# Kernel tuning notes

Measured on AMD Instinct MI355X. Metric: run time of the kernel, lower is better.

Reference implementation:

```python
import jax, jax.numpy as jnp
import numpy as np

DIM = 128
HEADS = 4
HD = DIM // HEADS  # 32
WS = 8             # search window (ws x ws candidates)
K = 16             # top-k neighbors kept
SCALE = HD ** -0.5


def _sepconv(x, w_dw, w_pw, b):
    # depthwise 3x3 ('SAME', reflect-free) + pointwise 1x1 with bias (SepConv2d)
    C = x.shape[1]
    y = jax.lax.conv_general_dilated(x, w_dw, (1, 1), 'SAME',
                                     feature_group_count=C,
                                     dimension_numbers=('NCHW', 'OIHW', 'NCHW'))
    return jnp.einsum('bchw,oc->bohw', y, w_pw) + b[None, :, None, None]


def _refl(i, n):
    # dnls reflect_bounds: mirror indices back into [0, n-1]
    i = jnp.where(i < 0, -i, i)
    return jnp.where(i >= n, 2 * (n - 1) - i, i)


def _neighbor_idx(T, H, W, ws):
    # flat pixel index of the ws*ws spatial candidates per query (wt=0: same frame)
    off = jnp.arange(ws) - ws // 2
    ni = _refl(jnp.arange(H)[:, None] + off[None, :], H)  # [H,ws]
    nj = _refl(jnp.arange(W)[:, None] + off[None, :], W)  # [W,ws]
    pix = ni[:, None, :, None] * W + nj[None, :, None, :]  # [H,W,ws,ws]
    idx = jnp.arange(T)[:, None, None, None, None] * (H * W) + pix[None]
    return idx.reshape(T * H * W, ws * ws).astype(jnp.int32)  # [Q,L]


def reference(vid, wq_dw, wq_pw, bq, wk_dw, wk_pw, bk, wv_dw, wv_pw, bv, proj_w, proj_b):
    B, T, C, H, W = vid.shape
    Q = T * H * W
    x = vid.reshape(B * T, C, H, W)
    # qkv conv projection; q pre-scaled as in get_qkv
    q = _sepconv(x, wq_dw, wq_pw, bq) * SCALE
    k = _sepconv(x, wk_dw, wk_pw, bk)
    v = _sepconv(x, wv_dw, wv_pw, bv)

    def heads(z):  # [B*T,C,H,W] -> [B,heads,Q,hd]
        return z.reshape(B, T, HEADS, HD, H, W).transpose(0, 2, 1, 4, 5, 3).reshape(B, HEADS, Q, HD)

    qh, kh, vh = heads(q), heads(k), heads(v)
    idx = _neighbor_idx(T, H, W, WS)            # [Q,L]
    kg = jnp.take(kh, idx, axis=2)              # [B,h,Q,L,hd] irregular gather
    dists = jnp.einsum('bhqd,bhqld->bhql', qh, kg)
    vals, args = jax.lax.top_k(dists, K)        # k-NN by prod distance
    attn = jax.nn.softmax(vals, axis=-1)        # run_softmax over k
    sel = jnp.take_along_axis(jnp.broadcast_to(idx[None, None], (B, HEADS) + idx.shape), args, axis=-1)
    vsel = jnp.take_along_axis(vh, sel.reshape(B, HEADS, Q * K)[..., None], axis=2).reshape(B, HEADS, Q, K, HD)
    out = jnp.einsum('bhqk,bhqkd->bhqd', attn, vsel)   # wpsum (ps=pt=1)
    out = out.transpose(0, 2, 1, 3).reshape(B, Q, C)   # merge heads: (h c)
    y = out @ proj_w.T + proj_b                        # nn.Linear proj
    # fold: ps=1, stride0=1 -> zvid==1, pure reshape back to video
    return y.reshape(B, T, H, W, C).transpose(0, 1, 4, 2, 3)


def setup_inputs() -> dict:
    key = jax.random.key(0)
    ks = jax.random.split(key, 12)
    s = 0.02
    return {
        'vid': jax.random.normal(ks[0], (1, 2, DIM, 96, 96), jnp.float32),
        'wq_dw': jax.random.normal(ks[1], (DIM, 1, 3, 3), jnp.float32) * s,
        'wq_pw': jax.random.normal(ks[2], (DIM, DIM), jnp.float32) * s,
        'bq': jax.random.normal(ks[3], (DIM,), jnp.float32) * s,
        'wk_dw': jax.random.normal(ks[4], (DIM, 1, 3, 3), jnp.float32) * s,
        'wk_pw': jax.random.normal(ks[5], (DIM, DIM), jnp.float32) * s,
        'bk': jax.random.normal(ks[6], (DIM,), jnp.float32) * s,
        'wv_dw': jax.random.normal(ks[7], (DIM, 1, 3, 3), jnp.float32) * s,
        'wv_pw': jax.random.normal(ks[8], (DIM, DIM), jnp.float32) * s,
        'bv': jax.random.normal(ks[9], (DIM,), jnp.float32) * s,
        'proj_w': jax.random.normal(ks[10], (DIM, DIM), jnp.float32) * s,
        'proj_b': jax.random.normal(ks[11], (DIM,), jnp.float32) * s,
    }
```

## Files before the change

kernel.cpp:

```cpp
#include <hip/hip_runtime.h>
#include <math.h>

#define TT 2
#define CH 128
#define HH 96
#define WW 96
#define HWS 9216
#define QTOT 18432
#define QC (QTOT*CH)
#define HD 32
#define KTOP 16
#define SCALE 0.17677669529663687f

#define SEG 16
#define PR 8
#define PC 23
#define PSTRIDE 36

typedef __attribute__((ext_vector_type(8))) short short8;
typedef __attribute__((ext_vector_type(4))) float floatx4;

__device__ __forceinline__ unsigned short f2bf(float f) {
    union { float f; unsigned u; } x; x.f = f;
    unsigned r = x.u + 0x7fffu + ((x.u >> 16) & 1u);
    return (unsigned short)(r >> 16);
}
__device__ __forceinline__ float bf2f(unsigned short h) {
    return __uint_as_float(((unsigned)h) << 16);
}

__device__ __forceinline__ int refl(int x, int n) {
    x = x < 0 ? -x : x;
    return x >= n ? 2 * (n - 1) - x : x;
}

__global__ __launch_bounds__(256) void dw_kernel(
    const float* __restrict__ x,
    const float* __restrict__ wq, const float* __restrict__ wk, const float* __restrict__ wv,
    float* __restrict__ t_dw)
{
    int tid = blockIdx.x * 256 + threadIdx.x;
    int hw = tid % HWS;
    int cf = tid / HWS;
    int c = cf & (CH - 1);
    int tt = cf >> 7;
    int i = hw / WW, j = hw % WW;
    const float* xp = x + (size_t)(tt * CH + c) * HWS;
    float w0[9], w1[9], w2[9];
#pragma unroll
    for (int r = 0; r < 9; r++) { w0[r] = wq[c * 9 + r]; w1[r] = wk[c * 9 + r]; w2[r] = wv[c * 9 + r]; }
    float s0 = 0.f, s1 = 0.f, s2 = 0.f;
#pragma unroll
    for (int r = 0; r < 3; r++) {
        int ii = i + r - 1;
        if (ii < 0 || ii >= HH) continue;
#pragma unroll
        for (int ss = 0; ss < 3; ss++) {
            int jj = j + ss - 1;
            if (jj < 0 || jj >= WW) continue;
            float xv = xp[ii * WW + jj];
            s0 += xv * w0[r * 3 + ss];
            s1 += xv * w1[r * 3 + ss];
            s2 += xv * w2[r * 3 + ss];
        }
    }
    size_t o = (size_t)c * QTOT + tt * HWS + hw;
    t_dw[o] = s0;
    t_dw[QC + o] = s1;
    t_dw[2 * (size_t)QC + o] = s2;
}

__global__ __launch_bounds__(256) void transcvt(
    const float* __restrict__ t_dw,
    unsigned short* __restrict__ qk_hi,
    unsigned short* __restrict__ qk_lo,
    unsigned short* __restrict__ v_bf)
{
    __shared__ float s[64][33];
    int sel = blockIdx.z;
    const float* vd = t_dw + (size_t)sel * QC;
    int t = threadIdx.x;
    int p0 = blockIdx.x * 64;
    int c0 = blockIdx.y * 32;
#pragma unroll
    for (int r = 0; r < 2; r++) {
        int lin = r * 256 + t;
        int c = lin >> 4;
        int pq = lin & 15;
        float4 v4 = *(const float4*)(vd + (size_t)(c0 + c) * QTOT + p0 + pq * 4);
        s[pq * 4 + 0][c] = v4.x; s[pq * 4 + 1][c] = v4.y;
        s[pq * 4 + 2][c] = v4.z; s[pq * 4 + 3][c] = v4.w;
    }
    __syncthreads();
    int p = t >> 2, cq = t & 3;
    unsigned uh[8], ul[8];
#pragma unroll
    for (int j = 0; j < 8; j++) {
        float x = s[p][cq * 8 + j];
        unsigned short h = f2bf(x);
        uh[j] = h;
        ul[j] = f2bf(x - bf2f(h));
    }
    uint4 ph, pl;
    ph.x = uh[0] | (uh[1] << 16); ph.y = uh[2] | (uh[3] << 16);
    ph.z = uh[4] | (uh[5] << 16); ph.w = uh[6] | (uh[7] << 16);
    size_t off = (size_t)(p0 + p) * CH + c0 + cq * 8;
    if (sel < 2) {
        pl.x = ul[0] | (ul[1] << 16); pl.y = ul[2] | (ul[3] << 16);
        pl.z = ul[4] | (ul[5] << 16); pl.w = ul[6] | (ul[7] << 16);
        *(uint4*)(qk_hi + (size_t)sel * QC + off) = ph;
        *(uint4*)(qk_lo + (size_t)sel * QC + off) = pl;
    } else {
        *(uint4*)(v_bf + off) = ph;
    }
}

__global__ __launch_bounds__(256) void qk_mfma(
    const unsigned short* __restrict__ Ahi,
    const unsigned short* __restrict__ Alo,
    const float* __restrict__ wq_pw, const float* __restrict__ wk_pw,
    const float* __restrict__ bq, const float* __restrict__ bk,
    float* __restrict__ t_dw)
{
    int sel = blockIdx.y;
    const float* W = sel ? wk_pw : wq_pw;
    const float* bias = sel ? bk : bq;
    float scale = sel ? 1.f : SCALE;
    const unsigned short* ah = Ahi + (size_t)sel * QC;
    const unsigned short* al = Alo + (size_t)sel * QC;
    float* O = t_dw + (size_t)sel * QC;

    __shared__ unsigned short Wh[128 * 136];
    __shared__ unsigned short Wl[128 * 136];
    int t = threadIdx.x;
#pragma unroll
    for (int r = 0; r < 16; r++) {
        int lin = r * 256 + t;
        int o = lin >> 5, cq = lin & 31;
        float4 w4 = *(const float4*)(W + o * CH + cq * 4);
        unsigned short hx = f2bf(w4.x), hy = f2bf(w4.y), hz = f2bf(w4.z), hw = f2bf(w4.w);
        unsigned short lx = f2bf(w4.x - bf2f(hx)), ly = f2bf(w4.y - bf2f(hy));
        unsigned short lz = f2bf(w4.z - bf2f(hz)), lw = f2bf(w4.w - bf2f(hw));
        uint2 pk;
        pk.x = hx | ((unsigned)hy << 16); pk.y = hz | ((unsigned)hw << 16);
        *(uint2*)(&Wh[o * 136 + cq * 4]) = pk;
        pk.x = lx | ((unsigned)ly << 16); pk.y = lz | ((unsigned)lw << 16);
        *(uint2*)(&Wl[o * 136 + cq * 4]) = pk;
    }
    __syncthreads();
    int wv = t >> 6, lane = t & 63;
    int m = lane & 15, quad = lane >> 4;
    int p0 = blockIdx.x * 64;
    int o0 = wv * 32;
    float bb[2];
#pragma unroll
    for (int ot = 0; ot < 2; ot++) bb[ot] = bias[o0 + ot * 16 + m];
    floatx4 acc[4][2];
#pragma unroll
    for (int i = 0; i < 4; i++)
#pragma unroll
        for (int j = 0; j < 2; j++) acc[i][j] = (floatx4){0.f, 0.f, 0.f, 0.f};
#pragma unroll
    for (int kc = 0; kc < 4; kc++) {
        short8 avh[4], avl[4], bh[2], bl[2];
#pragma unroll
        for (int pt = 0; pt < 4; pt++) {
            size_t base = (size_t)(p0 + pt * 16 + m) * CH + kc * 32 + quad * 8;
            avh[pt] = *(const short8*)(ah + base);
            avl[pt] = *(const short8*)(al + base);
        }
#pragma unroll
        for (int ot = 0; ot < 2; ot++) {
            int lidx = (o0 + ot * 16 + m) * 136 + kc * 32 + quad * 8;
            bh[ot] = *(const short8*)(&Wh[lidx]);
            bl[ot] = *(const short8*)(&Wl[lidx]);
        }
#pragma unroll
        for (int pt = 0; pt < 4; pt++)
#pragma unroll
            for (int ot = 0; ot < 2; ot++) {
                acc[pt][ot] = __builtin_amdgcn_mfma_f32_16x16x32_bf16(avh[pt], bh[ot], acc[pt][ot], 0, 0, 0);
                acc[pt][ot] = __builtin_amdgcn_mfma_f32_16x16x32_bf16(avh[pt], bl[ot], acc[pt][ot], 0, 0, 0);
                acc[pt][ot] = __builtin_amdgcn_mfma_f32_16x16x32_bf16(avl[pt], bh[ot], acc[pt][ot], 0, 0, 0);
            }
    }
#pragma unroll
    for (int pt = 0; pt < 4; pt++)
#pragma unroll
        for (int ot = 0; ot < 2; ot++)
#pragma unroll
            for (int reg = 0; reg < 4; reg++) {
                int p = p0 + pt * 16 + quad * 4 + reg;
                O[(size_t)p * CH + o0 + ot * 16 + m] = (acc[pt][ot][reg] + bb[ot]) * scale;
            }
}

__global__ __launch_bounds__(256) void vgemm_mfma(
    const unsigned short* __restrict__ A,
    const float* __restrict__ W,
    const float* __restrict__ bias,
    float* __restrict__ O)
{
    __shared__ unsigned short Ws[128 * 136];
    int t = threadIdx.x;
#pragma unroll
    for (int r = 0; r < 16; r++) {
        int lin = r * 256 + t;
        int o = lin >> 5, cq = lin & 31;
        float4 w4 = *(const float4*)(W + o * CH + cq * 4);
        uint2 pk;
        pk.x = f2bf(w4.x) | ((unsigned)f2bf(w4.y) << 16);
        pk.y = f2bf(w4.z) | ((unsigned)f2bf(w4.w) << 16);
        *(uint2*)(&Ws[o * 136 + cq * 4]) = pk;
    }
    __syncthreads();
    int wv = t >> 6, lane = t & 63;
    int m = lane & 15, quad = lane >> 4;
    int p0 = blockIdx.x * 64;
    int o0 = wv * 32;
    float bb[2];
#pragma unroll
    for (int ot = 0; ot < 2; ot++) bb[ot] = bias[o0 + ot * 16 + m];
    floatx4 acc[4][2];
#pragma unroll
    for (int i = 0; i < 4; i++)
#pragma unroll
        for (int j = 0; j < 2; j++) acc[i][j] = (floatx4){0.f, 0.f, 0.f, 0.f};
#pragma unroll
    for (int kc = 0; kc < 4; kc++) {
        short8 a[4], b[2];
#pragma unroll
        for (int pt = 0; pt < 4; pt++)
            a[pt] = *(const short8*)(A + (size_t)(p0 + pt * 16 + m) * CH + kc * 32 + quad * 8);
#pragma unroll
        for (int ot = 0; ot < 2; ot++)
            b[ot] = *(const short8*)(&Ws[(o0 + ot * 16 + m) * 136 + kc * 32 + quad * 8]);
#pragma unroll
        for (int pt = 0; pt < 4; pt++)
#pragma unroll
            for (int ot = 0; ot < 2; ot++)
                acc[pt][ot] = __builtin_amdgcn_mfma_f32_16x16x32_bf16(a[pt], b[ot], acc[pt][ot], 0, 0, 0);
    }
#pragma unroll
    for (int pt = 0; pt < 4; pt++)
#pragma unroll
        for (int ot = 0; ot < 2; ot++)
#pragma unroll
            for (int reg = 0; reg < 4; reg++) {
                int p = p0 + pt * 16 + quad * 4 + reg;
                O[(size_t)p * CH + o0 + ot * 16 + m] = acc[pt][ot][reg] + bb[ot];
            }
}

__global__ __launch_bounds__(256) void attn_kernel(
    const float* __restrict__ q,
    const float* __restrict__ k,
    const float* __restrict__ v,
    unsigned short* __restrict__ att)
{
    __shared__ float kp[PR * PC * PSTRIDE];
    int h = blockIdx.y;
    int seg = blockIdx.x;
    int qj0 = (seg % (WW / SEG)) * SEG;
    int qi = (seg / (WW / SEG)) % HH;
    int tt = seg / ((WW / SEG) * HH);
    int t = threadIdx.x;

#pragma unroll
    for (int r = 0; r < 6; r++) {
        int f = r * 256 + t;
        if (f < PR * PC * 8) {
            int pix = f >> 3, d4 = f & 7;
            int ci = pix / PC, cj = pix - ci * PC;
            int gi = refl(qi + ci - 4, HH);
            int gj = refl(qj0 + cj - 4, WW);
            int gp = tt * HWS + gi * WW + gj;
            *(float4*)(&kp[pix * PSTRIDE + d4 * 4]) =
                *(const float4*)(k + (size_t)gp * CH + h * HD + d4 * 4);
        }
    }
    __syncthreads();

    int wv = t >> 6, lane = t & 63;
    int ci = lane >> 3, cjo = lane & 7;
    int di = ci - 4, dj = cjo - 4;
    int rowoff = tt * HWS + refl(qi + di, HH) * WW;
    const int d = lane & (HD - 1);
    const unsigned long long below = (1ull << lane) - 1ull;

    for (int ql = wv * 4; ql < wv * 4 + 4; ql++) {
        int qj = qj0 + ql;
        int p = tt * HWS + qi * WW + qj;
        const float* qp = q + (size_t)p * CH + h * HD;
        const float* kr = &kp[(ci * PC + ql + cjo) * PSTRIDE];
        float dist = 0.f;
#pragma unroll
        for (int dd = 0; dd < 8; dd++) {
            float4 qv = *(const float4*)(qp + dd * 4);
            float4 kv = *(const float4*)(kr + dd * 4);
            dist += qv.x * kv.x + qv.y * kv.y + qv.z * kv.z + qv.w * kv.w;
        }
        int cpix = rowoff + refl(qj + dj, WW);

        unsigned u = __float_as_uint(dist);
        unsigned key = (u & 0x80000000u) ? ~u : (u | 0x80000000u);

        unsigned prefix = 0u;
        int need = KTOP;
#pragma unroll
        for (int bit = 31; bit >= 0; --bit) {
            unsigned hi = (prefix >> bit) | 1u;
            unsigned long long b = __ballot((key >> bit) == hi);
            int cnt = __popcll(b);
            bool take = cnt >= need;
            prefix = take ? (prefix | (1u << bit)) : prefix;
            need = take ? need : need - cnt;
        }
        bool isEq = (key == prefix);
        unsigned long long eqm = __ballot(isEq);
        int rk = __popcll(eqm & below);
        bool selb = (key > prefix) || (isEq && rk < need);
        unsigned long long selm = __ballot(selb);

        float e = selb ? __expf(dist) : 0.f;

        float acc = 0.f, denom = 0.f;
        unsigned long long m0 = selm;
#pragma unroll
        for (int r = 0; r < KTOP; r++) {
            int s0 = __builtin_ctzll(m0); m0 &= m0 - 1ull;
            float a0 = __uint_as_float((unsigned)__builtin_amdgcn_readlane((int)__float_as_uint(e), s0));
            int p0 = __builtin_amdgcn_readlane(cpix, s0);
            denom += a0;
            acc += a0 * v[(size_t)p0 * CH + h * HD + d];
        }
        if (lane < HD)
            att[(size_t)p * CH + h * HD + lane] = f2bf(acc / denom);
    }
}

__global__ __launch_bounds__(256) void proj_mfma(
    const unsigned short* __restrict__ A,
    const float* __restrict__ W,
    const float* __restrict__ bias,
    float* __restrict__ out)
{
    __shared__ unsigned short Ws[128 * 136];
    int t = threadIdx.x;
#pragma unroll
    for (int r = 0; r < 16; r++) {
        int lin = r * 256 + t;
        int o = lin >> 5, cq = lin & 31;
        float4 w4 = *(const float4*)(W + o * CH + cq * 4);
        uint2 pk;
        pk.x = f2bf(w4.x) | ((unsigned)f2bf(w4.y) << 16);
        pk.y = f2bf(w4.z) | ((unsigned)f2bf(w4.w) << 16);
        *(uint2*)(&Ws[o * 136 + cq * 4]) = pk;
    }
    __syncthreads();
    int wv = t >> 6, lane = t & 63;
    int m = lane & 15, quad = lane >> 4;
    int p0 = blockIdx.x * 64;
    int o0 = wv * 32;
    float bb[2][4];
#pragma unroll
    for (int ot = 0; ot < 2; ot++)
#pragma unroll
        for (int reg = 0; reg < 4; reg++) bb[ot][reg] = bias[o0 + ot * 16 + quad * 4 + reg];
    floatx4 acc[2][4];
#pragma unroll
    for (int i = 0; i < 2; i++)
#pragma unroll
        for (int j = 0; j < 4; j++) acc[i][j] = (floatx4){0.f, 0.f, 0.f, 0.f};
#pragma unroll
    for (int kc = 0; kc < 4; kc++) {
        short8 a[2], b[4];
#pragma unroll
        for (int ot = 0; ot < 2; ot++)
            a[ot] = *(const short8*)(&Ws[(o0 + ot * 16 + m) * 136 + kc * 32 + quad * 8]);
#pragma unroll
        for (int pt = 0; pt < 4; pt++)
            b[pt] = *(const short8*)(A + (size_t)(p0 + pt * 16 + m) * CH + kc * 32 + quad * 8);
#pragma unroll
        for (int ot = 0; ot < 2; ot++)
#pragma unroll
            for (int pt = 0; pt < 4; pt++)
                acc[ot][pt] = __builtin_amdgcn_mfma_f32_16x16x32_bf16(a[ot], b[pt], acc[ot][pt], 0, 0, 0);
    }
    int tt = p0 / HWS;
    int hwb = p0 - tt * HWS;
#pragma unroll
    for (int ot = 0; ot < 2; ot++)
#pragma unroll
        for (int pt = 0; pt < 4; pt++)
#pragma unroll
            for (int reg = 0; reg < 4; reg++) {
                int o = o0 + ot * 16 + quad * 4 + reg;
                int hw = hwb + pt * 16 + m;
                out[((size_t)(tt * CH + o)) * HWS + hw] = acc[ot][pt][reg] + bb[ot][reg];
            }
}

extern "C" void kernel_launch(void* const* d_in, const int* in_sizes, int n_in,
                              void* d_out, int out_size, void* d_ws, size_t ws_size,
                              hipStream_t stream) {
    const float* vid    = (const float*)d_in[0];
    const float* wq_dw  = (const float*)d_in[1];
    const float* wq_pw  = (const float*)d_in[2];
    const float* bq     = (const float*)d_in[3];
    const float* wk_dw  = (const float*)d_in[4];
    const float* wk_pw  = (const float*)d_in[5];
    const float* bk     = (const float*)d_in[6];
    const float* wv_dw  = (const float*)d_in[7];
    const float* wv_pw  = (const float*)d_in[8];
    const float* bv     = (const float*)d_in[9];
    const float* proj_w = (const float*)d_in[10];
    const float* proj_b = (const float*)d_in[11];
    float* out = (float*)d_out;

    float* t_dw = (float*)d_ws;
    float* v_f32 = t_dw + (size_t)3 * QC;
    unsigned short* qk_hi = (unsigned short*)(v_f32 + (size_t)QC);
    unsigned short* qk_lo = qk_hi + (size_t)2 * QC;
    unsigned short* v_bf = qk_lo + (size_t)2 * QC;
    unsigned short* att_bf = v_bf;

    dw_kernel<<<QTOT * CH / 256, 256, 0, stream>>>(vid, wq_dw, wk_dw, wv_dw, t_dw);
    transcvt<<<dim3(QTOT / 64, 4, 3), 256, 0, stream>>>(t_dw, qk_hi, qk_lo, v_bf);
    qk_mfma<<<dim3(QTOT / 64, 2), 256, 0, stream>>>(qk_hi, qk_lo, wq_pw, wk_pw, bq, bk, t_dw);
    vgemm_mfma<<<QTOT / 64, 256, 0, stream>>>(v_bf, wv_pw, bv, v_f32);
    attn_kernel<<<dim3(TT * HH * (WW / SEG), 4), 256, 0, stream>>>(
        t_dw, t_dw + (size_t)QC, v_f32, att_bf);
    proj_mfma<<<QTOT / 64, 256, 0, stream>>>(att_bf, proj_w, proj_b, out);
}
```

Measured before the change: 205.8 us.

## Precompute bf16 weight splits once and give attention one wave per query

A new wprep kernel converts the four pointwise and projection weight matrices to bf16 (with hi/lo splits for q and k) once per call into workspace. The GEMM kernels then read those weights straight from global memory instead of having every block convert them into LDS. Separately, the attention kernel now runs 1024-thread blocks with one wave per query instead of each wave looping over four queries, which raises parallelism. The cost is an extra kernel launch, uncached global weight reads inside the MFMA loops, and lower occupancy headroom from the larger blocks.

```diff
diff --git a/kernel.cpp b/kernel.cpp
--- a/kernel.cpp
+++ b/kernel.cpp
@@ -17,6 +17,10 @@
 #define PC 23
 #define PSTRIDE 36
 
+#define WB_QK(sel) ((sel) * 32768)
+#define WB_V 65536
+#define WB_P 81920
+
 typedef __attribute__((ext_vector_type(8))) short short8;
 typedef __attribute__((ext_vector_type(4))) float floatx4;
 
@@ -32,6 +36,28 @@
 __device__ __forceinline__ int refl(int x, int n) {
     x = x < 0 ? -x : x;
     return x >= n ? 2 * (n - 1) - x : x;
+}
+
+__global__ __launch_bounds__(256) void wprep(
+    const float* __restrict__ wq, const float* __restrict__ wk,
+    const float* __restrict__ wv, const float* __restrict__ pj,
+    unsigned short* __restrict__ wbuf)
+{
+    int sel = blockIdx.y;
+    const float* src = sel == 0 ? wq : (sel == 1 ? wk : (sel == 2 ? wv : pj));
+    int hi_off = sel == 0 ? 0 : (sel == 1 ? 32768 : (sel == 2 ? WB_V : WB_P));
+    int idx = blockIdx.x * 256 + threadIdx.x;
+    float4 w4 = *(const float4*)(src + idx * 4);
+    unsigned short hx = f2bf(w4.x), hy = f2bf(w4.y), hz = f2bf(w4.z), hw = f2bf(w4.w);
+    uint2 pk;
+    pk.x = hx | ((unsigned)hy << 16); pk.y = hz | ((unsigned)hw << 16);
+    *(uint2*)(wbuf + hi_off + idx * 4) = pk;
+    if (sel < 2) {
+        unsigned short lx = f2bf(w4.x - bf2f(hx)), ly = f2bf(w4.y - bf2f(hy));
+        unsigned short lz = f2bf(w4.z - bf2f(hz)), lw = f2bf(w4.w - bf2f(hw));
+        pk.x = lx | ((unsigned)ly << 16); pk.y = lz | ((unsigned)lw << 16);
+        *(uint2*)(wbuf + hi_off + 16384 + idx * 4) = pk;
+    }
 }
 
 __global__ __launch_bounds__(256) void dw_kernel(
@@ -118,36 +144,20 @@
 __global__ __launch_bounds__(256) void qk_mfma(
     const unsigned short* __restrict__ Ahi,
     const unsigned short* __restrict__ Alo,
-    const float* __restrict__ wq_pw, const float* __restrict__ wk_pw,
+    const unsigned short* __restrict__ wbuf,
     const float* __restrict__ bq, const float* __restrict__ bk,
     float* __restrict__ t_dw)
 {
     int sel = blockIdx.y;
-    const float* W = sel ? wk_pw : wq_pw;
+    const unsigned short* Wh = wbuf + WB_QK(sel);
+    const unsigned short* Wl = Wh + 16384;
     const float* bias = sel ? bk : bq;
     float scale = sel ? 1.f : SCALE;
     const unsigned short* ah = Ahi + (size_t)sel * QC;
     const unsigned short* al = Alo + (size_t)sel * QC;
     float* O = t_dw + (size_t)sel * QC;
 
-    __shared__ unsigned short Wh[128 * 136];
-    __shared__ unsigned short Wl[128 * 136];
     int t = threadIdx.x;
-#pragma unroll
-    for (int r = 0; r < 16; r++) {
-        int lin = r * 256 + t;
-        int o = lin >> 5, cq = lin & 31;
-        float4 w4 = *(const float4*)(W + o * CH + cq * 4);
-        unsigned short hx = f2bf(w4.x), hy = f2bf(w4.y), hz = f2bf(w4.z), hw = f2bf(w4.w);
-        unsigned short lx = f2bf(w4.x - bf2f(hx)), ly = f2bf(w4.y - bf2f(hy));
-        unsigned short lz = f2bf(w4.z - bf2f(hz)), lw = f2bf(w4.w - bf2f(hw));
-        uint2 pk;
-        pk.x = hx | ((unsigned)hy << 16); pk.y = hz | ((unsigned)hw << 16);
-        *(uint2*)(&Wh[o * 136 + cq * 4]) = pk;
-        pk.x = lx | ((unsigned)ly << 16); pk.y = lz | ((unsigned)lw << 16);
-        *(uint2*)(&Wl[o * 136 + cq * 4]) = pk;
-    }
-    __syncthreads();
     int wv = t >> 6, lane = t & 63;
     int m = lane & 15, quad = lane >> 4;
     int p0 = blockIdx.x * 64;
@@ -171,9 +181,9 @@
         }
 #pragma unroll
         for (int ot = 0; ot < 2; ot++) {
-            int lidx = (o0 + ot * 16 + m) * 136 + kc * 32 + quad * 8;
-            bh[ot] = *(const short8*)(&Wh[lidx]);
-            bl[ot] = *(const short8*)(&Wl[lidx]);
+            int widx = (o0 + ot * 16 + m) * CH + kc * 32 + quad * 8;
+            bh[ot] = *(const short8*)(Wh + widx);
+            bl[ot] = *(const short8*)(Wl + widx);
         }
 #pragma unroll
         for (int pt = 0; pt < 4; pt++)
@@ -197,23 +207,12 @@
 
 __global__ __launch_bounds__(256) void vgemm_mfma(
     const unsigned short* __restrict__ A,
-    const float* __restrict__ W,
+    const unsigned short* __restrict__ wbuf,
     const float* __restrict__ bias,
     float* __restrict__ O)
 {
-    __shared__ unsigned short Ws[128 * 136];
+    const unsigned short* Wv = wbuf + WB_V;
     int t = threadIdx.x;
-#pragma unroll
-    for (int r = 0; r < 16; r++) {
-        int lin = r * 256 + t;
-        int o = lin >> 5, cq = lin & 31;
-        float4 w4 = *(const float4*)(W + o * CH + cq * 4);
-        uint2 pk;
-        pk.x = f2bf(w4.x) | ((unsigned)f2bf(w4.y) << 16);
-        pk.y = f2bf(w4.z) | ((unsigned)f2bf(w4.w) << 16);
-        *(uint2*)(&Ws[o * 136 + cq * 4]) = pk;
-    }
-    __syncthreads();
     int wv = t >> 6, lane = t & 63;
     int m = lane & 15, quad = lane >> 4;
     int p0 = blockIdx.x * 64;
@@ -234,7 +233,7 @@
             a[pt] = *(const short8*)(A + (size_t)(p0 + pt * 16 + m) * CH + kc * 32 + quad * 8);
 #pragma unroll
         for (int ot = 0; ot < 2; ot++)
-            b[ot] = *(const short8*)(&Ws[(o0 + ot * 16 + m) * 136 + kc * 32 + quad * 8]);
+            b[ot] = *(const short8*)(Wv + (o0 + ot * 16 + m) * CH + kc * 32 + quad * 8);
 #pragma unroll
         for (int pt = 0; pt < 4; pt++)
 #pragma unroll
@@ -252,7 +251,7 @@
             }
 }
 
-__global__ __launch_bounds__(256) void attn_kernel(
+__global__ __launch_bounds__(1024) void attn_kernel(
     const float* __restrict__ q,
     const float* __restrict__ k,
     const float* __restrict__ v,
@@ -267,8 +266,8 @@
     int t = threadIdx.x;
 
 #pragma unroll
-    for (int r = 0; r < 6; r++) {
-        int f = r * 256 + t;
+    for (int r = 0; r < 2; r++) {
+        int f = r * 1024 + t;
         if (f < PR * PC * 8) {
             int pix = f >> 3, d4 = f & 7;
             int ci = pix / PC, cj = pix - ci * PC;
@@ -281,83 +280,70 @@
     }
     __syncthreads();
 
-    int wv = t >> 6, lane = t & 63;
+    int lane = t & 63;
+    int ql = __builtin_amdgcn_readfirstlane(t >> 6);
     int ci = lane >> 3, cjo = lane & 7;
     int di = ci - 4, dj = cjo - 4;
-    int rowoff = tt * HWS + refl(qi + di, HH) * WW;
     const int d = lane & (HD - 1);
     const unsigned long long below = (1ull << lane) - 1ull;
 
-    for (int ql = wv * 4; ql < wv * 4 + 4; ql++) {
-        int qj = qj0 + ql;
-        int p = tt * HWS + qi * WW + qj;
-        const float* qp = q + (size_t)p * CH + h * HD;
-        const float* kr = &kp[(ci * PC + ql + cjo) * PSTRIDE];
-        float dist = 0.f;
-#pragma unroll
-        for (int dd = 0; dd < 8; dd++) {
-            float4 qv = *(const float4*)(qp + dd * 4);
-            float4 kv = *(const float4*)(kr + dd * 4);
-            dist += qv.x * kv.x + qv.y * kv.y + qv.z * kv.z + qv.w * kv.w;
-        }
-        int cpix = rowoff + refl(qj + dj, WW);
-
-        unsigned u = __float_as_uint(dist);
-        unsigned key = (u & 0x80000000u) ? ~u : (u | 0x80000000u);
-
-        unsigned prefix = 0u;
-        int need = KTOP;
-#pragma unroll
-        for (int bit = 31; bit >= 0; --bit) {
-            unsigned hi = (prefix >> bit) | 1u;
-            unsigned long long b = __ballot((key >> bit) == hi);
-            int cnt = __popcll(b);
-            bool take = cnt >= need;
-            prefix = take ? (prefix | (1u << bit)) : prefix;
-            need = take ? need : need - cnt;
-        }
-        bool isEq = (key == prefix);
-        unsigned long long eqm = __ballot(isEq);
-        int rk = __popcll(eqm & below);
-        bool selb = (key > prefix) || (isEq && rk < need);
-        unsigned long long selm = __ballot(selb);
-
-        float e = selb ? __expf(dist) : 0.f;
-
-        float acc = 0.f, denom = 0.f;
-        unsigned long long m0 = selm;
-#pragma unroll
-        for (int r = 0; r < KTOP; r++) {
-            int s0 = __builtin_ctzll(m0); m0 &= m0 - 1ull;
-            float a0 = __uint_as_float((unsigned)__builtin_amdgcn_readlane((int)__float_as_uint(e), s0));
-            int p0 = __builtin_amdgcn_readlane(cpix, s0);
-            denom += a0;
-            acc += a0 * v[(size_t)p0 * CH + h * HD + d];
-        }
-        if (lane < HD)
-            att[(size_t)p * CH + h * HD + lane] = f2bf(acc / denom);
-    }
+    int qj = qj0 + ql;
+    int p = tt * HWS + qi * WW + qj;
+    const float* qp = q + (size_t)p * CH + h * HD;
+    const float* kr = &kp[(ci * PC + ql + cjo) * PSTRIDE];
+    float dist = 0.f;
+#pragma unroll
+    for (int dd = 0; dd < 8; dd++) {
+        float4 qv = *(const float4*)(qp + dd * 4);
+        float4 kv = *(const float4*)(kr + dd * 4);
+        dist += qv.x * kv.x + qv.y * kv.y + qv.z * kv.z + qv.w * kv.w;
+    }
+    int cpix = tt * HWS + refl(qi + di, HH) * WW + refl(qj + dj, WW);
+
+    unsigned u = __float_as_uint(dist);
+    unsigned key = (u & 0x80000000u) ? ~u : (u | 0x80000000u);
+
+    unsigned prefix = 0u;
+    int need = KTOP;
+#pragma unroll
+    for (int bit = 31; bit >= 0; --bit) {
+        unsigned hi = (prefix >> bit) | 1u;
+        unsigned long long b = __ballot((key >> bit) == hi);
+        int cnt = __popcll(b);
+        bool take = cnt >= need;
+        prefix = take ? (prefix | (1u << bit)) : prefix;
+        need = take ? need : need - cnt;
+    }
+    bool isEq = (key == prefix);
+    unsigned long long eqm = __ballot(isEq);
+    int rk = __popcll(eqm & below);
+    bool selb = (key > prefix) || (isEq && rk < need);
+    unsigned long long selm = __ballot(selb);
+
+    float e = selb ? __expf(dist) : 0.f;
+
+    float acc = 0.f, denom = 0.f;
+    unsigned long long m0 = selm;
+#pragma unroll
+    for (int r = 0; r < KTOP; r++) {
+        int s0 = __builtin_ctzll(m0); m0 &= m0 - 1ull;
+        float a0 = __uint_as_float((unsigned)__builtin_amdgcn_readlane((int)__float_as_uint(e), s0));
+        int pr = __builtin_amdgcn_readlane(cpix, s0);
+        denom += a0;
+        acc += a0 * v[(size_t)pr * CH + h * HD + d];
+    }
+    if (lane < HD)
+        att[(size_t)p * CH + h * HD + lane] = f2bf(acc / denom);
 }
 
 __global__ __launch_bounds__(256) void proj_mfma(
     const unsigned short* __restrict__ A,
-    const float* __restrict__ W,
+    const unsigned short* __restrict__ wbuf,
     const float* __restrict__ bias,
     float* __restrict__ out)
 {
-    __shared__ unsigned short Ws[128 * 136];
+    const unsigned short* Wp = wbuf + WB_P;
     int t = threadIdx.x;
-#pragma unroll
-    for (int r = 0; r < 16; r++) {
-        int lin = r * 256 + t;
-        int o = lin >> 5, cq = lin & 31;
-        float4 w4 = *(const float4*)(W + o * CH + cq * 4);
-        uint2 pk;
-        pk.x = f2bf(w4.x) | ((unsigned)f2bf(w4.y) << 16);
-        pk.y = f2bf(w4.z) | ((unsigned)f2bf(w4.w) << 16);
-        *(uint2*)(&Ws[o * 136 + cq * 4]) = pk;
-    }
-    __syncthreads();
     int wv = t >> 6, lane = t & 63;
     int m = lane & 15, quad = lane >> 4;
     int p0 = blockIdx.x * 64;
@@ -377,7 +363,7 @@
         short8 a[2], b[4];
 #pragma unroll
         for (int ot = 0; ot < 2; ot++)
-            a[ot] = *(const short8*)(&Ws[(o0 + ot * 16 + m) * 136 + kc * 32 + quad * 8]);
+            a[ot] = *(const short8*)(Wp + (o0 + ot * 16 + m) * CH + kc * 32 + quad * 8);
 #pragma unroll
         for (int pt = 0; pt < 4; pt++)
             b[pt] = *(const short8*)(A + (size_t)(p0 + pt * 16 + m) * CH + kc * 32 + quad * 8);
@@ -423,13 +409,15 @@
     unsigned short* qk_hi = (unsigned short*)(v_f32 + (size_t)QC);
     unsigned short* qk_lo = qk_hi + (size_t)2 * QC;
     unsigned short* v_bf = qk_lo + (size_t)2 * QC;
+    unsigned short* wbuf = v_bf + (size_t)QC;
     unsigned short* att_bf = v_bf;
 
+    wprep<<<dim3(16, 4), 256, 0, stream>>>(wq_pw, wk_pw, wv_pw, proj_w, wbuf);
     dw_kernel<<<QTOT * CH / 256, 256, 0, stream>>>(vid, wq_dw, wk_dw, wv_dw, t_dw);
     transcvt<<<dim3(QTOT / 64, 4, 3), 256, 0, stream>>>(t_dw, qk_hi, qk_lo, v_bf);
-    qk_mfma<<<dim3(QTOT / 64, 2), 256, 0, stream>>>(qk_hi, qk_lo, wq_pw, wk_pw, bq, bk, t_dw);
-    vgemm_mfma<<<QTOT / 64, 256, 0, stream>>>(v_bf, wv_pw, bv, v_f32);
-    attn_kernel<<<dim3(TT * HH * (WW / SEG), 4), 256, 0, stream>>>(
+    qk_mfma<<<dim3(QTOT / 64, 2), 256, 0, stream>>>(qk_hi, qk_lo, wbuf, bq, bk, t_dw);
+    vgemm_mfma<<<QTOT / 64, 256, 0, stream>>>(v_bf, wbuf, bv, v_f32);
+    attn_kernel<<<dim3(TT * HH * (WW / SEG), 4), 1024, 0, stream>>>(
         t_dw, t_dw + (size_t)QC, v_f32, att_bf);
-    proj_mfma<<<QTOT / 64, 256, 0, stream>>>(att_bf, proj_w, proj_b, out);
-}
+    proj_mfma<<<QTOT / 64, 256, 0, stream>>>(att_bf, wbuf, proj_b, out);
+}
```

Result: slower. 214.6 us (+4.3%).
